# Optimization experiments

Measured on AMD Instinct MI355X. Metric: run time of the kernel, lower is better.

Reference implementation:

```python
import jax, jax.numpy as jnp
import numpy as np

B, N, D, H = 2, 2048, 2048, 16
HD = D // H  # head_dim = 128
EPS = 1e-06

def rmsnorm(x, w, eps=EPS):
    xf = x.astype(jnp.float32)
    y = xf * jax.lax.rsqrt(jnp.mean(xf * xf, axis=-1, keepdims=True) + eps)
    return y.astype(x.dtype) * w

def rope_apply(x, freqs, num_heads):
    # x: [B, S, D]; freqs: [S, 1, HD//2, 2] = (cos, sin) of complex rotation
    b, s, d = x.shape
    hd = d // num_heads
    xr = x.reshape(b, s, num_heads, hd // 2, 2)
    x0, x1 = xr[..., 0], xr[..., 1]
    fr, fi = freqs[..., 0], freqs[..., 1]  # broadcast [S,1,HD//2] over heads
    out = jnp.stack([x0 * fr - x1 * fi, x0 * fi + x1 * fr], axis=-1)
    return out.reshape(b, s, d).astype(x.dtype)

def attention(q, k, v, num_heads):
    b, s, d = q.shape
    hd = d // num_heads
    qh = q.reshape(b, s, num_heads, hd).transpose(0, 2, 1, 3)  # b h s d
    kh = k.reshape(b, s, num_heads, hd).transpose(0, 2, 1, 3)
    vh = v.reshape(b, s, num_heads, hd).transpose(0, 2, 1, 3)
    scale = hd ** -0.5
    scores = jnp.einsum('bhqd,bhkd->bhqk', qh, kh) * scale
    probs = jax.nn.softmax(scores, axis=-1)
    out = jnp.einsum('bhqk,bhkd->bhqd', probs, vh)
    return out.transpose(0, 2, 1, 3).reshape(b, s, d)

def setup_inputs() -> dict:
    key = jax.random.key(0)
    ks = jax.random.split(key, 8)
    x = jax.random.normal(ks[0], (B, N, D), jnp.float32)
    # standard RoPE frequencies
    pos = jnp.arange(N, dtype=jnp.float32)
    inv = 1.0 / (10000.0 ** (jnp.arange(0, HD, 2, dtype=jnp.float32) / HD))
    ang = pos[:, None] * inv[None, :]  # [N, HD//2]
    freqs = jnp.stack([jnp.cos(ang), jnp.sin(ang)], axis=-1)[:, None, :, :]  # [N,1,HD//2,2]
    s = 0.02
    wq = jax.random.normal(ks[1], (D, D), jnp.float32) * s
    wk = jax.random.normal(ks[2], (D, D), jnp.float32) * s
    wv = jax.random.normal(ks[3], (D, D), jnp.float32) * s
    wo = jax.random.normal(ks[4], (D, D), jnp.float32) * s
    bq = jnp.zeros((D,), jnp.float32)
    bk = jnp.zeros((D,), jnp.float32)
    bv = jnp.zeros((D,), jnp.float32)
    bo = jnp.zeros((D,), jnp.float32)
    gq = jnp.ones((D,), jnp.float32)
    gk = jnp.ones((D,), jnp.float32)
    return {"x": x, "freqs": freqs, "wq": wq, "bq": bq, "wk": wk, "bk": bk,
            "wv": wv, "bv": bv, "wo": wo, "bo": bo, "gq": gq, "gk": gk}

def reference(x, freqs, wq, bq, wk, bk, wv, bv, wo, bo, gq, gk):
    q = rmsnorm(x @ wq.T + bq, gq)
    k = rmsnorm(x @ wk.T + bk, gk)
    v = x @ wv.T + bv
    q = rope_apply(q, freqs, H)
    k = rope_apply(k, freqs, H)
    attn_out = attention(q, k, v, H)
    return attn_out @ wo.T + bo
```

## Files before the change

kernel.cpp:

```cpp
#include <hip/hip_runtime.h>
#include <hip/hip_bf16.h>
#include <stdint.h>


typedef __bf16 bf16;
typedef __bf16 bf16x8 __attribute__((ext_vector_type(8)));
typedef __bf16 bf16x4 __attribute__((ext_vector_type(4)));
typedef float  f32x4  __attribute__((ext_vector_type(4)));
typedef float  f32x16 __attribute__((ext_vector_type(16)));
typedef unsigned int uint2v __attribute__((ext_vector_type(2)));

#define MTOT   4096
#define DMODEL 2048
#define NSEQ   2048
#define NHEAD  16
#define HDIM   128

static __device__ __forceinline__ void async_ld16(const void* g, void* l) {
  void* gnc = const_cast<void*>(g);
  __builtin_amdgcn_global_load_lds((__attribute__((address_space(1))) void*)gnc,
                                   (__attribute__((address_space(3))) void*)l,
                                   16, 0, 0);
}

#define XG (MTOT * DMODEL / 8)
#define WG (DMODEL * DMODEL / 8)

__global__ __launch_bounds__(256) void k_cvt4(
    const float* __restrict__ x, const float* __restrict__ wq,
    const float* __restrict__ wk, const float* __restrict__ wv,
    bf16* __restrict__ xb, bf16* __restrict__ wqb, bf16* __restrict__ wkb,
    bf16* __restrict__ wvb) {
  int stride = gridDim.x * blockDim.x;
  for (int i = blockIdx.x * blockDim.x + threadIdx.x; i < XG + 3 * WG;
       i += stride) {
    const float* src;
    bf16* dst;
    int off;
    if (i < XG) { src = x; dst = xb; off = i; }
    else if (i < XG + WG) { src = wq; dst = wqb; off = i - XG; }
    else if (i < XG + 2 * WG) { src = wk; dst = wkb; off = i - XG - WG; }
    else { src = wv; dst = wvb; off = i - XG - 2 * WG; }
    const float4* p = (const float4*)(src) + 2 * (size_t)off;
    float4 a = p[0], b = p[1];
    bf16x8 o;
    o[0] = (bf16)a.x; o[1] = (bf16)a.y; o[2] = (bf16)a.z; o[3] = (bf16)a.w;
    o[4] = (bf16)b.x; o[5] = (bf16)b.y; o[6] = (bf16)b.z; o[7] = (bf16)b.w;
    *((bf16x8*)(dst) + off) = o;
  }
}

__global__ __launch_bounds__(256) void k_cvt(const float* __restrict__ in,
                                             bf16* __restrict__ out, int n8) {
  int stride = gridDim.x * blockDim.x;
  for (int i = blockIdx.x * blockDim.x + threadIdx.x; i < n8; i += stride) {
    const float4* p = (const float4*)(in) + 2 * (size_t)i;
    float4 a = p[0], b = p[1];
    bf16x8 o;
    o[0] = (bf16)a.x; o[1] = (bf16)a.y; o[2] = (bf16)a.z; o[3] = (bf16)a.w;
    o[4] = (bf16)b.x; o[5] = (bf16)b.y; o[6] = (bf16)b.z; o[7] = (bf16)b.w;
    *((bf16x8*)(out) + i) = o;
  }
}

#define BUFELEMS (384 * 64)

template <int OUTMODE>
static __device__ __forceinline__ void gemm256_body(
    const bf16* __restrict__ A, const bf16* __restrict__ W,
    const float* __restrict__ bias, void* __restrict__ outp, int m0, int n0) {
  extern __shared__ __align__(16) bf16 dynls[];

  const int tid = threadIdx.x;
  const int lane = tid & 63, w = tid >> 6;
  const int wm = w >> 2, wn = w & 3;
  const int g = lane >> 4, r0 = lane & 15;

  f32x4 acc[4][4];
  const f32x4 vzero = {0.f, 0.f, 0.f, 0.f};
#pragma unroll
  for (int i = 0; i < 4; ++i)
#pragma unroll
    for (int j = 0; j < 4; ++j) acc[i][j] = vzero;

  const bf16* Abase = A + (size_t)m0 * DMODEL;
  const bf16* Wbase = W + (size_t)n0 * DMODEL;

  auto stage_a = [&](int kt, int buf) {
    const bf16* asrc = Abase + kt * 64;
    const bf16* bsrc = Wbase + kt * 64;
    bf16* sBuf = dynls + buf * BUFELEMS;
#pragma unroll
    for (int p = 0; p < 2; ++p) {
      int ch = tid + p * 512;
      int row = ch >> 3, c = (ch & 7) ^ (row & 7);
      async_ld16(asrc + (size_t)row * DMODEL + c * 8, sBuf + ch * 8);
    }
    {
      int ch = tid;
      int row = ch >> 3, c = (ch & 7) ^ (row & 7);
      async_ld16(bsrc + (size_t)row * DMODEL + c * 8, sBuf + 128 * 64 + ch * 8);
    }
  };
  auto stage_b = [&](int kt, int buf) {
    const bf16* bsrc = Wbase + kt * 64;
    bf16* sBuf = dynls + buf * BUFELEMS + 128 * 64;
#pragma unroll
    for (int p = 1; p < 4; ++p) {
      int ch = tid + p * 512;
      int row = ch >> 3, c = (ch & 7) ^ (row & 7);
      async_ld16(bsrc + (size_t)row * DMODEL + c * 8, sBuf + ch * 8);
    }
  };

  const int NT = DMODEL / 64;
  stage_a(0, 0); stage_b(0, 0);
  stage_a(1, 1); stage_b(1, 1);
  asm volatile("s_waitcnt vmcnt(6)" ::: "memory");
  __builtin_amdgcn_s_barrier();

  for (int kt = 0; kt < NT; ++kt) {
    const bf16* sA = dynls + (kt % 3) * BUFELEMS;
    const bf16* sB = sA + 128 * 64;
    const bool pf = (kt + 2) < NT;
    const int nb = (kt + 2) % 3;

#pragma unroll
    for (int ks = 0; ks < 2; ++ks) {
      bf16x8 af[4], bfr[4];
      const int cc = ks * 4 + g;
#pragma unroll
      for (int i = 0; i < 4; ++i) {
        int ra = wm * 64 + i * 16 + r0;
        af[i] = *(const bf16x8*)(sA + ra * 64 + ((cc ^ (ra & 7)) << 3));
        int rb = wn * 64 + i * 16 + r0;
        bfr[i] = *(const bf16x8*)(sB + rb * 64 + ((cc ^ (rb & 7)) << 3));
      }
      if (ks == 0) {
        if (pf) stage_a(kt + 2, nb);
      } else {
        if (pf) {
          stage_b(kt + 2, nb);
          asm volatile("s_waitcnt vmcnt(6)" ::: "memory");
        } else {
          asm volatile("s_waitcnt vmcnt(0)" ::: "memory");
        }
      }
      __builtin_amdgcn_sched_barrier(0);
      __builtin_amdgcn_s_barrier();
      __builtin_amdgcn_sched_barrier(0);
      __builtin_amdgcn_s_setprio(1);
#pragma unroll
      for (int i = 0; i < 4; ++i)
#pragma unroll
        for (int j = 0; j < 4; ++j)
          acc[i][j] = __builtin_amdgcn_mfma_f32_16x16x32_bf16(af[i], bfr[j],
                                                              acc[i][j], 0, 0, 0);
      __builtin_amdgcn_s_setprio(0);
    }
  }

#pragma unroll
  for (int i = 0; i < 4; ++i) {
#pragma unroll
    for (int j = 0; j < 4; ++j) {
      int mb = m0 + wm * 64 + i * 16 + g * 4;
      int n = n0 + wn * 64 + j * 16 + r0;
      float bn = bias[n];
      if (OUTMODE == 0) {
        bf16* o = (bf16*)outp;
#pragma unroll
        for (int r = 0; r < 4; ++r)
          o[(size_t)(mb + r) * DMODEL + n] = (bf16)(acc[i][j][r] + bn);
      } else if (OUTMODE == 2) {
        float* o = (float*)outp;
#pragma unroll
        for (int r = 0; r < 4; ++r)
          o[(size_t)(mb + r) * DMODEL + n] = acc[i][j][r] + bn;
      } else {
        bf16* o = (bf16*)outp;
        int bb = mb >> 11, s = mb & (NSEQ - 1);
        bf16x4 pk;
#pragma unroll
        for (int r = 0; r < 4; ++r) pk[r] = (bf16)(acc[i][j][r] + bn);
        *(bf16x4*)(o + (size_t)(bb * DMODEL + n) * NSEQ + s) = pk;
      }
    }
  }
}

__global__ __launch_bounds__(512, 2) void k_gemm_qkv(
    const bf16* __restrict__ xb, const bf16* __restrict__ wq,
    const bf16* __restrict__ wk, const bf16* __restrict__ wv,
    const float* __restrict__ bq, const float* __restrict__ bk,
    const float* __restrict__ bv, bf16* __restrict__ q, bf16* __restrict__ k,
    bf16* __restrict__ vt) {
  int nb = blockIdx.x;
  int m0 = blockIdx.y * 128;
  int sec = nb >> 3;
  int n0 = (nb & 7) * 256;
  if (sec == 0)
    gemm256_body<0>(xb, wq, bq, q, m0, n0);
  else if (sec == 1)
    gemm256_body<0>(xb, wk, bk, k, m0, n0);
  else
    gemm256_body<1>(xb, wv, bv, vt, m0, n0);
}

__global__ __launch_bounds__(512, 2) void k_gemm_out(
    const bf16* __restrict__ ab, const bf16* __restrict__ wo,
    const float* __restrict__ bo, float* __restrict__ out) {
  gemm256_body<2>(ab, wo, bo, out, blockIdx.y * 128, blockIdx.x * 256);
}

__global__ __launch_bounds__(256) void k_norm_rope(
    bf16* __restrict__ q, bf16* __restrict__ kk, const float* __restrict__ gq,
    const float* __restrict__ gk, const float* __restrict__ freqs) {
  int bidx = blockIdx.x;
  bf16* buf = (bidx < MTOT) ? q : kk;
  const float* gw = (bidx < MTOT) ? gq : gk;
  float qs = (bidx < MTOT) ? 0.08838834764831845f : 1.0f;
  int row = bidx & (MTOT - 1);
  int s = row & (NSEQ - 1);
  int tid = threadIdx.x;
  int i0 = tid * 8;
  bf16* ptr = buf + (size_t)row * DMODEL + i0;
  bf16x8 v = *(const bf16x8*)ptr;
  float x[8];
  float ssq = 0.f;
#pragma unroll
  for (int j = 0; j < 8; ++j) {
    x[j] = (float)v[j];
    ssq += x[j] * x[j];
  }
#pragma unroll
  for (int off = 1; off < 64; off <<= 1) ssq += __shfl_xor(ssq, off);
  __shared__ float part[4];
  if ((tid & 63) == 0) part[tid >> 6] = ssq;
  __syncthreads();
  float tot = part[0] + part[1] + part[2] + part[3];
  float sc = rsqrtf(tot * (1.f / DMODEL) + 1e-6f) * qs;
  float4 g0 = *(const float4*)(gw + i0);
  float4 g1 = *(const float4*)(gw + i0 + 4);
  float y[8];
  y[0] = x[0] * sc * g0.x; y[1] = x[1] * sc * g0.y;
  y[2] = x[2] * sc * g0.z; y[3] = x[3] * sc * g0.w;
  y[4] = x[4] * sc * g1.x; y[5] = x[5] * sc * g1.y;
  y[6] = x[6] * sc * g1.z; y[7] = x[7] * sc * g1.w;
  int dl = i0 & (HDIM - 1);
  const float* fp = freqs + (size_t)s * HDIM + dl;
  float4 f0 = *(const float4*)fp;
  float4 f1 = *(const float4*)(fp + 4);
  bf16x8 out;
  out[0] = (bf16)(y[0] * f0.x - y[1] * f0.y);
  out[1] = (bf16)(y[0] * f0.y + y[1] * f0.x);
  out[2] = (bf16)(y[2] * f0.z - y[3] * f0.w);
  out[3] = (bf16)(y[2] * f0.w + y[3] * f0.z);
  out[4] = (bf16)(y[4] * f1.x - y[5] * f1.y);
  out[5] = (bf16)(y[4] * f1.y + y[5] * f1.x);
  out[6] = (bf16)(y[6] * f1.z - y[7] * f1.w);
  out[7] = (bf16)(y[6] * f1.w + y[7] * f1.z);
  *(bf16x8*)ptr = out;
}

__global__ __launch_bounds__(256, 2) void k_attn(const bf16* __restrict__ q,
                                                 const bf16* __restrict__ k,
                                                 const bf16* __restrict__ vt,
                                                 bf16* __restrict__ o) {
  __shared__ __align__(16) bf16 sk[2][64 * 128];
  __shared__ __align__(16) bf16 sv[2][128 * 64];
  const int bid = blockIdx.x;
  const int idx = bid >> 3;
  const int bh = (bid & 7) * 4 + (idx >> 4);
  const int qt = idx & 15;
  const int bb = bh >> 4, h = bh & 15;
  const int tid = threadIdx.x;
  const int lane = tid & 63, w = tid >> 6;
  const int l31 = lane & 31, b5 = lane >> 5;

  bf16x8 qf[8];
  {
    const bf16* qb =
        q + (size_t)(bb * NSEQ + qt * 128 + w * 32 + l31) * DMODEL + h * HDIM +
        b5 * 8;
#pragma unroll
    for (int kk = 0; kk < 8; ++kk) qf[kk] = *(const bf16x8*)(qb + kk * 16);
  }

  f32x16 oacc[4];
#pragma unroll
  for (int dt = 0; dt < 4; ++dt)
#pragma unroll
    for (int r = 0; r < 16; ++r) oacc[dt][r] = 0.f;
  float m = -3.0e38f, l = 0.f;

  const bf16* kbase = k + (size_t)(bb * NSEQ) * DMODEL + h * HDIM;
  const bf16* vbase = vt + (size_t)(bb * DMODEL + h * HDIM) * NSEQ;

  auto stage = [&](int t, int buf) {
    int k0 = t * 64;
#pragma unroll
    for (int p = 0; p < 4; ++p) {
      int ch = tid + p * 256;
      int row = ch >> 4, cs = ch & 15;
      int c = cs ^ (row & 7);
      async_ld16(kbase + (size_t)(k0 + row) * DMODEL + c * 8, &sk[buf][ch * 8]);
    }
#pragma unroll
    for (int p = 0; p < 4; ++p) {
      int ch = tid + p * 256;
      int row = ch >> 3, cs = ch & 7;
      int c = cs ^ (row & 7);
      async_ld16(vbase + (size_t)row * NSEQ + k0 + c * 8, &sv[buf][ch * 8]);
    }
  };

  stage(0, 0);
  for (int t = 0; t < NSEQ / 64; ++t) {
    const int cur = t & 1;
    asm volatile("s_waitcnt vmcnt(0)" ::: "memory");
    __syncthreads();
    if (t + 1 < NSEQ / 64) stage(t + 1, cur ^ 1);

    f32x16 sacc[2];
#pragma unroll
    for (int s = 0; s < 2; ++s)
#pragma unroll
      for (int r = 0; r < 16; ++r) sacc[s][r] = 0.f;
#pragma unroll
    for (int s = 0; s < 2; ++s) {
      const int row = s * 32 + l31;
#pragma unroll
      for (int kk = 0; kk < 8; ++kk) {
        const int c = 2 * kk + b5;
        bf16x8 kf = *(const bf16x8*)(&sk[cur][row * 128 + ((c ^ (row & 7)) << 3)]);
        sacc[s] = __builtin_amdgcn_mfma_f32_32x32x16_bf16(kf, qf[kk], sacc[s],
                                                          0, 0, 0);
      }
    }

    float t1[8];
#pragma unroll
    for (int i = 0; i < 8; ++i)
      t1[i] = fmaxf(fmaxf(sacc[0][2 * i], sacc[0][2 * i + 1]),
                    fmaxf(sacc[1][2 * i], sacc[1][2 * i + 1]));
    float pm = fmaxf(fmaxf(fmaxf(t1[0], t1[1]), fmaxf(t1[2], t1[3])),
                     fmaxf(fmaxf(t1[4], t1[5]), fmaxf(t1[6], t1[7])));
    {
      uint2v r2 = __builtin_amdgcn_permlane32_swap(__float_as_uint(pm),
                                                   __float_as_uint(pm), false,
                                                   false);
      pm = fmaxf(__uint_as_float(r2.x), __uint_as_float(r2.y));
    }
    const int need = __any(pm > m + 8.0f);
    if (need) {
      float mn = fmaxf(m, pm);
      float alpha = __expf(m - mn);
      m = mn;
      l *= alpha;
#pragma unroll
      for (int dt = 0; dt < 4; ++dt)
#pragma unroll
        for (int r = 0; r < 16; ++r) oacc[dt][r] *= alpha;
    }

    float rs = 0.f;
#pragma unroll
    for (int s = 0; s < 2; ++s)
#pragma unroll
      for (int r = 0; r < 16; ++r) {
        float pv = __expf(sacc[s][r] - m);
        sacc[s][r] = pv;
        rs += pv;
      }
    {
      uint2v r2 = __builtin_amdgcn_permlane32_swap(__float_as_uint(rs),
                                                   __float_as_uint(rs), false,
                                                   false);
      rs = __uint_as_float(r2.x) + __uint_as_float(r2.y);
    }
    l += rs;

    uint32_t P2[16];
#pragma unroll
    for (int s = 0; s < 2; ++s)
#pragma unroll
      for (int i = 0; i < 8; ++i)
        asm("v_cvt_pk_bf16_f32 %0, %1, %2"
            : "=v"(P2[s * 8 + i])
            : "v"(sacc[s][2 * i]), "v"(sacc[s][2 * i + 1]));

#pragma unroll
    for (int s = 0; s < 2; ++s) {
#pragma unroll
      for (int u = 0; u < 2; ++u) {
        union { uint32_t uw[4]; bf16x8 v; } pb;
        uint2v ra = __builtin_amdgcn_permlane32_swap(P2[s * 8 + 4 * u],
                                                     P2[s * 8 + 4 * u + 2],
                                                     false, false);
        uint2v rb = __builtin_amdgcn_permlane32_swap(P2[s * 8 + 4 * u + 1],
                                                     P2[s * 8 + 4 * u + 3],
                                                     false, false);
        pb.uw[0] = ra.x;
        pb.uw[1] = rb.x;
        pb.uw[2] = ra.y;
        pb.uw[3] = rb.y;
        const int c = 4 * s + 2 * u + b5;
#pragma unroll
        for (int dt = 0; dt < 4; ++dt) {
          const int rv = dt * 32 + l31;
          bf16x8 vf =
              *(const bf16x8*)(&sv[cur][rv * 64 + ((c ^ (rv & 7)) << 3)]);
          oacc[dt] = __builtin_amdgcn_mfma_f32_32x32x16_bf16(vf, pb.v, oacc[dt],
                                                             0, 0, 0);
        }
      }
    }
  }

  const float rl = 1.f / l;
  bf16* ob = o + (size_t)(bb * NSEQ + qt * 128 + w * 32 + l31) * DMODEL +
             h * HDIM;
#pragma unroll
  for (int dt = 0; dt < 4; ++dt) {
#pragma unroll
    for (int rg = 0; rg < 4; ++rg) {
      bf16x4 pk4;
#pragma unroll
      for (int e = 0; e < 4; ++e) pk4[e] = (bf16)(oacc[dt][rg * 4 + e] * rl);
      *(bf16x4*)(ob + dt * 32 + rg * 8 + b5 * 4) = pk4;
    }
  }
}

extern "C" void kernel_launch(void* const* d_in, const int* in_sizes, int n_in,
                              void* d_out, int out_size, void* d_ws,
                              size_t ws_size, hipStream_t stream) {
  (void)in_sizes; (void)n_in; (void)out_size; (void)ws_size;
  const float* x = (const float*)d_in[0];
  const float* freqs = (const float*)d_in[1];
  const float* wq = (const float*)d_in[2];
  const float* bq = (const float*)d_in[3];
  const float* wk = (const float*)d_in[4];
  const float* bk = (const float*)d_in[5];
  const float* wv = (const float*)d_in[6];
  const float* bv = (const float*)d_in[7];
  const float* wo = (const float*)d_in[8];
  const float* bo = (const float*)d_in[9];
  const float* gq = (const float*)d_in[10];
  const float* gk = (const float*)d_in[11];

  char* ws = (char*)d_ws;
  const size_t SZ_TOK = (size_t)MTOT * DMODEL * sizeof(bf16);
  const size_t SZ_W = (size_t)DMODEL * DMODEL * sizeof(bf16);
  bf16* xb = (bf16*)ws;
  bf16* qb = (bf16*)(ws + SZ_TOK);
  bf16* kb = (bf16*)(ws + 2 * SZ_TOK);
  bf16* vtb = (bf16*)(ws + 3 * SZ_TOK);
  bf16* wqb = (bf16*)(ws + 4 * SZ_TOK);
  bf16* wkb = (bf16*)(ws + 4 * SZ_TOK + SZ_W);
  bf16* wvb = (bf16*)(ws + 4 * SZ_TOK + 2 * SZ_W);

  const int LDSB = 3 * BUFELEMS * (int)sizeof(bf16);
  hipFuncSetAttribute((const void*)k_gemm_qkv,
                      hipFuncAttributeMaxDynamicSharedMemorySize, LDSB);
  hipFuncSetAttribute((const void*)k_gemm_out,
                      hipFuncAttributeMaxDynamicSharedMemorySize, LDSB);

  k_cvt4<<<2048, 256, 0, stream>>>(x, wq, wk, wv, xb, wqb, wkb, wvb);

  k_gemm_qkv<<<dim3(24, 32), 512, LDSB, stream>>>(xb, wqb, wkb, wvb, bq, bk,
                                                  bv, qb, kb, vtb);
  k_cvt<<<1024, 256, 0, stream>>>(wo, wqb, (DMODEL * DMODEL) / 8);

  k_norm_rope<<<2 * MTOT, 256, 0, stream>>>(qb, kb, gq, gk, freqs);

  k_attn<<<512, 256, 0, stream>>>(qb, kb, vtb, xb);

  k_gemm_out<<<dim3(8, 32), 512, LDSB, stream>>>(xb, wqb, bo, (float*)d_out);
}
```

Before: 270.2 us.

## Split QKV GEMM into 256x256-tile Q/K kernel and separate V kernel

```diff
diff --git a/kernel.cpp b/kernel.cpp
--- a/kernel.cpp
+++ b/kernel.cpp
@@ -63,6 +63,162 @@
   }
 }
 
+__global__ __launch_bounds__(512, 2) void k_gemm_qk(
+    const bf16* __restrict__ xb, const bf16* __restrict__ wq,
+    const bf16* __restrict__ wk, const float* __restrict__ bq,
+    const float* __restrict__ bk, bf16* __restrict__ q, bf16* __restrict__ k) {
+  extern __shared__ __align__(16) bf16 dyn[];
+
+  const int swz = (blockIdx.x & 7) * 32 + (blockIdx.x >> 3);
+  const int mt = swz >> 4, nt = swz & 15;
+  const int sec = nt >> 3;
+  const int m0 = mt * 256, n0 = (nt & 7) * 256;
+  const bf16* W = sec ? wk : wq;
+  const float* bias = sec ? bk : bq;
+  bf16* outp = sec ? k : q;
+
+  const int tid = threadIdx.x;
+  const int lane = tid & 63, w = tid >> 6;
+  const int wm = w >> 2, wn = w & 3;
+  const int g = lane >> 4, r0 = lane & 15;
+
+  f32x4 acc[8][4];
+  const f32x4 vzero = {0.f, 0.f, 0.f, 0.f};
+#pragma unroll
+  for (int i = 0; i < 8; ++i)
+#pragma unroll
+    for (int j = 0; j < 4; ++j) acc[i][j] = vzero;
+
+  const bf16* Abase = xb + (size_t)m0 * DMODEL;
+  const bf16* Wbase = W + (size_t)n0 * DMODEL;
+
+  auto stage = [&](int kt, int buf) {
+    const bf16* asrc = Abase + kt * 64;
+    const bf16* bsrc = Wbase + kt * 64;
+    bf16* sA = dyn + buf * 32768;
+    bf16* sB = sA + 16384;
+#pragma unroll
+    for (int p = 0; p < 4; ++p) {
+      int ch = tid + p * 512;
+      int row = ch >> 3, c = (ch & 7) ^ (row & 7);
+      async_ld16(asrc + (size_t)row * DMODEL + c * 8, sA + ch * 8);
+    }
+#pragma unroll
+    for (int p = 0; p < 4; ++p) {
+      int ch = tid + p * 512;
+      int row = ch >> 3, c = (ch & 7) ^ (row & 7);
+      async_ld16(bsrc + (size_t)row * DMODEL + c * 8, sB + ch * 8);
+    }
+  };
+
+  const int NT = DMODEL / 64;
+  stage(0, 0);
+  for (int kt = 0; kt < NT; ++kt) {
+    const int cur = kt & 1;
+    if (kt > 0) __builtin_amdgcn_s_barrier();
+    if (kt + 1 < NT) {
+      stage(kt + 1, cur ^ 1);
+      asm volatile("s_waitcnt vmcnt(8)" ::: "memory");
+    } else {
+      asm volatile("s_waitcnt vmcnt(0)" ::: "memory");
+    }
+    __builtin_amdgcn_s_barrier();
+    const bf16* sA = dyn + cur * 32768;
+    const bf16* sB = sA + 16384;
+
+    bf16x8 a0[8], a1[8], b0[4], b1[4];
+#pragma unroll
+    for (int i = 0; i < 4; ++i) {
+      int ra = wm * 128 + i * 16 + r0;
+#pragma unroll
+      for (int ks = 0; ks < 2; ++ks) {
+        int cc = ks * 4 + g;
+        a0[i * 2 + ks] = *(const bf16x8*)(sA + ra * 64 + ((cc ^ (ra & 7)) << 3));
+      }
+    }
+#pragma unroll
+    for (int j = 0; j < 2; ++j) {
+      int rb = wn * 64 + j * 16 + r0;
+#pragma unroll
+      for (int ks = 0; ks < 2; ++ks) {
+        int cc = ks * 4 + g;
+        b0[j * 2 + ks] = *(const bf16x8*)(sB + rb * 64 + ((cc ^ (rb & 7)) << 3));
+      }
+    }
+#pragma unroll
+    for (int j = 0; j < 2; ++j) {
+      int rb = wn * 64 + 32 + j * 16 + r0;
+#pragma unroll
+      for (int ks = 0; ks < 2; ++ks) {
+        int cc = ks * 4 + g;
+        b1[j * 2 + ks] = *(const bf16x8*)(sB + rb * 64 + ((cc ^ (rb & 7)) << 3));
+      }
+    }
+    __builtin_amdgcn_s_setprio(1);
+#pragma unroll
+    for (int i = 0; i < 4; ++i)
+#pragma unroll
+      for (int j = 0; j < 2; ++j)
+#pragma unroll
+        for (int ks = 0; ks < 2; ++ks)
+          acc[i][j] = __builtin_amdgcn_mfma_f32_16x16x32_bf16(
+              a0[i * 2 + ks], b0[j * 2 + ks], acc[i][j], 0, 0, 0);
+    __builtin_amdgcn_s_setprio(0);
+#pragma unroll
+    for (int i = 0; i < 4; ++i) {
+      int ra = wm * 128 + 64 + i * 16 + r0;
+#pragma unroll
+      for (int ks = 0; ks < 2; ++ks) {
+        int cc = ks * 4 + g;
+        a1[i * 2 + ks] = *(const bf16x8*)(sA + ra * 64 + ((cc ^ (ra & 7)) << 3));
+      }
+    }
+    __builtin_amdgcn_s_setprio(1);
+#pragma unroll
+    for (int i = 0; i < 4; ++i)
+#pragma unroll
+      for (int j = 0; j < 2; ++j)
+#pragma unroll
+        for (int ks = 0; ks < 2; ++ks)
+          acc[i][2 + j] = __builtin_amdgcn_mfma_f32_16x16x32_bf16(
+              a0[i * 2 + ks], b1[j * 2 + ks], acc[i][2 + j], 0, 0, 0);
+    __builtin_amdgcn_s_setprio(0);
+    __builtin_amdgcn_s_setprio(1);
+#pragma unroll
+    for (int i = 0; i < 4; ++i)
+#pragma unroll
+      for (int j = 0; j < 2; ++j)
+#pragma unroll
+        for (int ks = 0; ks < 2; ++ks)
+          acc[4 + i][j] = __builtin_amdgcn_mfma_f32_16x16x32_bf16(
+              a1[i * 2 + ks], b0[j * 2 + ks], acc[4 + i][j], 0, 0, 0);
+    __builtin_amdgcn_s_setprio(0);
+    __builtin_amdgcn_s_setprio(1);
+#pragma unroll
+    for (int i = 0; i < 4; ++i)
+#pragma unroll
+      for (int j = 0; j < 2; ++j)
+#pragma unroll
+        for (int ks = 0; ks < 2; ++ks)
+          acc[4 + i][2 + j] = __builtin_amdgcn_mfma_f32_16x16x32_bf16(
+              a1[i * 2 + ks], b1[j * 2 + ks], acc[4 + i][2 + j], 0, 0, 0);
+    __builtin_amdgcn_s_setprio(0);
+  }
+
+#pragma unroll
+  for (int i = 0; i < 8; ++i) {
+#pragma unroll
+    for (int j = 0; j < 4; ++j) {
+      int mb = m0 + wm * 128 + (i >> 2) * 64 + (i & 3) * 16 + g * 4;
+      int n = n0 + wn * 64 + (j >> 1) * 32 + (j & 1) * 16 + r0;
+      float bn = bias[n];
+#pragma unroll
+      for (int r = 0; r < 4; ++r)
+        outp[(size_t)(mb + r) * DMODEL + n] = (bf16)(acc[i][j][r] + bn);
+    }
+  }
+}
+
 #define BUFELEMS (384 * 64)
 
 template <int OUTMODE>
@@ -189,22 +345,10 @@
   }
 }
 
-__global__ __launch_bounds__(512, 2) void k_gemm_qkv(
-    const bf16* __restrict__ xb, const bf16* __restrict__ wq,
-    const bf16* __restrict__ wk, const bf16* __restrict__ wv,
-    const float* __restrict__ bq, const float* __restrict__ bk,
-    const float* __restrict__ bv, bf16* __restrict__ q, bf16* __restrict__ k,
-    bf16* __restrict__ vt) {
-  int nb = blockIdx.x;
-  int m0 = blockIdx.y * 128;
-  int sec = nb >> 3;
-  int n0 = (nb & 7) * 256;
-  if (sec == 0)
-    gemm256_body<0>(xb, wq, bq, q, m0, n0);
-  else if (sec == 1)
-    gemm256_body<0>(xb, wk, bk, k, m0, n0);
-  else
-    gemm256_body<1>(xb, wv, bv, vt, m0, n0);
+__global__ __launch_bounds__(512, 2) void k_gemm_v(
+    const bf16* __restrict__ xb, const bf16* __restrict__ wv,
+    const float* __restrict__ bv, bf16* __restrict__ vt) {
+  gemm256_body<1>(xb, wv, bv, vt, blockIdx.y * 128, blockIdx.x * 256);
 }
 
 __global__ __launch_bounds__(512, 2) void k_gemm_out(
@@ -462,15 +606,19 @@
   bf16* wvb = (bf16*)(ws + 4 * SZ_TOK + 2 * SZ_W);
 
   const int LDSB = 3 * BUFELEMS * (int)sizeof(bf16);
-  hipFuncSetAttribute((const void*)k_gemm_qkv,
+  const int LDSQK = 2 * 32768 * (int)sizeof(bf16);
+  hipFuncSetAttribute((const void*)k_gemm_qk,
+                      hipFuncAttributeMaxDynamicSharedMemorySize, LDSQK);
+  hipFuncSetAttribute((const void*)k_gemm_v,
                       hipFuncAttributeMaxDynamicSharedMemorySize, LDSB);
   hipFuncSetAttribute((const void*)k_gemm_out,
                       hipFuncAttributeMaxDynamicSharedMemorySize, LDSB);
 
   k_cvt4<<<2048, 256, 0, stream>>>(x, wq, wk, wv, xb, wqb, wkb, wvb);
 
-  k_gemm_qkv<<<dim3(24, 32), 512, LDSB, stream>>>(xb, wqb, wkb, wvb, bq, bk,
-                                                  bv, qb, kb, vtb);
+  k_gemm_qk<<<256, 512, LDSQK, stream>>>(xb, wqb, wkb, bq, bk, qb, kb);
+  k_gemm_v<<<dim3(8, 32), 512, LDSB, stream>>>(xb, wvb, bv, vtb);
+
   k_cvt<<<1024, 256, 0, stream>>>(wo, wqb, (DMODEL * DMODEL) / 8);
 
   k_norm_rope<<<2 * MTOT, 256, 0, stream>>>(qb, kb, gq, gk, freqs);
```

Result: faster. 263.3 us (-2.6%).
